# Optimization experiments

Hardware: AMD Instinct MI355X
Metric: run time of the kernel (lower is better)

Reference implementation:

```python
import jax, jax.numpy as jnp
import numpy as np

B = 8192          # batch of scenes
H = 20            # human_num
O = 10            # other_robot_num
IN = 13           # input_dim
SELF = 6          # self_state_dim
AG = IN - SELF    # agent_state_dim = 7
E1, E2 = 256, 128 # wr_dims / wh_dims
HID = 32          # hardcoded hidden_channels in Graphgnn
FIN = 128         # final_state_dim
P1, P2, P3 = 256, 128, 1  # planning_dims
NE = 8            # number of hetero edge types
# edge-type index convention:
# 0 robot->human, 1 human->robot, 2 other->robot, 3 robot->other,
# 4 other->human, 5 human->other, 6 human->human, 7 other->other


def setup_inputs() -> dict:
    key = jax.random.key(0)
    ks = iter(jax.random.split(key, 40))
    def nrm(shape, scale=0.05):
        return jax.random.normal(next(ks), shape, jnp.float32) * scale
    inp = {}
    inp["state"] = jax.random.normal(next(ks), (B, H + O, IN), jnp.float32)
    inp["dropout"] = 0  # unused by forward (kept for signature fidelity)
    # w_r: SELF -> E1 -> E2 (last_relu=True)
    inp["wr_W0"] = nrm((SELF, E1)); inp["wr_b0"] = nrm((E1,))
    inp["wr_W1"] = nrm((E1, E2));   inp["wr_b1"] = nrm((E2,))
    # w_h: AG -> E1 -> E2
    inp["wh_W0"] = nrm((AG, E1));   inp["wh_b0"] = nrm((E1,))
    inp["wh_W1"] = nrm((E1, E2));   inp["wh_b1"] = nrm((E2,))
    # w_o: AG -> E1 -> E2
    inp["wo_W0"] = nrm((AG, E1));   inp["wo_b0"] = nrm((E1,))
    inp["wo_W1"] = nrm((E1, E2));   inp["wo_b1"] = nrm((E2,))
    # per-edge-type GraphConv params (PyG GraphConv: lin_rel has bias, lin_root has none)
    inp["c1_relW"]  = nrm((NE, E2, HID)); inp["c1_relb"]  = nrm((NE, HID))
    inp["c1_rootW"] = nrm((NE, E2, HID))
    inp["c2_relW"]  = nrm((NE, HID, FIN)); inp["c2_relb"]  = nrm((NE, FIN))
    inp["c2_rootW"] = nrm((NE, HID, FIN))
    # value_net: FIN -> P1 -> P2 -> P3 (no final relu)
    inp["v_W0"] = nrm((FIN, P1)); inp["v_b0"] = nrm((P1,))
    inp["v_W1"] = nrm((P1, P2));  inp["v_b1"] = nrm((P2,))
    inp["v_W2"] = nrm((P2, P3));  inp["v_b2"] = nrm((P3,))
    return inp


def _mlp2(x, W0, b0, W1, b1, last_relu):
    h = jax.nn.relu(x @ W0 + b0)
    h = h @ W1 + b1
    return jax.nn.relu(h) if last_relu else h


def _hetero_conv(xr, xh, xo, relW, relb, rootW):
    # xr: [B,1,D], xh: [B,H,D], xo: [B,O,D]
    # GraphConv per edge type: out_dst = lin_root(x_dst) + lin_rel(sum of src messages)
    # graph is complete bipartite (sence) / complete-minus-self (affect),
    # so aggregations are closed-form sums.
    lin  = lambda x, i: jnp.einsum('bnd,do->bno', x, relW[i]) + relb[i]
    root = lambda x, i: jnp.einsum('bnd,do->bno', x, rootW[i])
    sh = xh.sum(axis=1, keepdims=True)  # [B,1,D] sum over humans
    so = xo.sum(axis=1, keepdims=True)  # [B,1,D] sum over other robots
    # robot receives: human->robot (1), other->robot (2)
    out_r = lin(sh, 1) + root(xr, 1) + lin(so, 2) + root(xr, 2)
    # human receives: robot->human (0), other->human (4), human->human (6)
    out_h = (lin(xr, 0) + root(xh, 0)
             + lin(so, 4) + root(xh, 4)
             + lin(sh - xh, 6) + root(xh, 6))
    # other receives: robot->other (3), human->other (5), other->other (7)
    out_o = (lin(xr, 3) + root(xo, 3)
             + lin(sh, 5) + root(xo, 5)
             + lin(so - xo, 7) + root(xo, 7))
    return out_r, out_h, out_o


def reference(state, dropout,
              wr_W0, wr_b0, wr_W1, wr_b1,
              wh_W0, wh_b0, wh_W1, wh_b1,
              wo_W0, wo_b0, wo_W1, wo_b1,
              c1_relW, c1_relb, c1_rootW,
              c2_relW, c2_relb, c2_rootW,
              v_W0, v_b0, v_W1, v_b1, v_W2, v_b2):
    self_state = state[:, 0, :SELF]          # [B, SELF]
    human_states = state[:, :H, SELF:]       # [B, H, AG]
    other_states = state[:, H:, SELF:]       # [B, O, AG]
    er = _mlp2(self_state, wr_W0, wr_b0, wr_W1, wr_b1, True)[:, None, :]  # [B,1,E2]
    eh = _mlp2(human_states, wh_W0, wh_b0, wh_W1, wh_b1, True)            # [B,H,E2]
    eo = _mlp2(other_states, wo_W0, wo_b0, wo_W1, wo_b1, True)            # [B,O,E2]
    r, h, o = _hetero_conv(er, eh, eo, c1_relW, c1_relb, c1_rootW)
    r, h, o = jax.nn.relu(r), jax.nn.relu(h), jax.nn.relu(o)
    r, h, o = _hetero_conv(r, h, o, c2_relW, c2_relb, c2_rootW)
    r = jax.nn.relu(r)
    hr = r[:, 0, :]                           # robot node per scene, [B, FIN]
    v = jax.nn.relu(hr @ v_W0 + v_b0)
    v = jax.nn.relu(v @ v_W1 + v_b1)
    v = v @ v_W2 + v_b2                       # [B, 1]
    return v
```

## Files before the change

kernel.cpp:

```cpp
#include <hip/hip_runtime.h>
#include <hip/hip_bf16.h>
#include <stdint.h>

#define BATCH 8192
#define NSTATE 30
#define DIN 13
#define E1 256
#define E2 128

typedef short bf16x8 __attribute__((ext_vector_type(8)));
typedef float f32x4 __attribute__((ext_vector_type(4)));

__device__ __forceinline__ unsigned short f2b(float f) {
    unsigned u = __float_as_uint(f);
    u += 0x7FFFu + ((u >> 16) & 1u);
    return (unsigned short)(u >> 16);
}
__device__ __forceinline__ float b2f(unsigned short b) {
    return __uint_as_float((unsigned)b << 16);
}
__device__ __forceinline__ unsigned pack2(float a, float b) {
    return ((unsigned)f2b(fmaxf(b, 0.f)) << 16) | f2b(fmaxf(a, 0.f));
}
__device__ __forceinline__ unsigned pack2n(float a, float b) {
    return ((unsigned)f2b(b) << 16) | f2b(a);
}

__device__ __forceinline__ float wcat_val(int k, int m, const float* relW, const float* rootW) {
    int part = k >> 7, c = k & 127, grp = m >> 5, mm = m & 31;
    int off = c * 32 + mm;
    if (part == 0) return (grp == 0) ? rootW[4096 + off] + rootW[8192 + off]
                        : (grp == 1) ? relW[off] : relW[3*4096 + off];
    if (part == 1) return (grp == 0) ? relW[1*4096 + off]
                        : (grp == 1) ? relW[6*4096 + off] : relW[5*4096 + off];
    return (grp == 0) ? relW[2*4096 + off]
         : (grp == 1) ? relW[4*4096 + off] : relW[7*4096 + off];
}
__device__ __forceinline__ float wc2_val(int k, int n, const float* relW, const float* rootW) {
    int grp = k >> 5, kk = k & 31;
    int off = kk * 128 + n;
    if (grp == 0) return rootW[4096 + off] + rootW[8192 + off];
    if (grp == 1) return relW[4096 + off];
    return relW[8192 + off];
}

__global__ void k_prep(const float* __restrict__ c1_relW, const float* __restrict__ c1_relb,
                       const float* __restrict__ c1_rootW,
                       const float* __restrict__ c2_relW, const float* __restrict__ c2_relb,
                       const float* __restrict__ c2_rootW,
                       const float* __restrict__ wh_W0, const float* __restrict__ wh_W1,
                       const float* __restrict__ wo_W0, const float* __restrict__ wo_W1,
                       const float* __restrict__ wr_W0, const float* __restrict__ wr_W1,
                       const float* __restrict__ v_W0, const float* __restrict__ v_W1,
                       float* __restrict__ bcat, float* __restrict__ bc2,
                       unsigned short* __restrict__ W0b_h, unsigned short* __restrict__ W0b_o,
                       unsigned short* __restrict__ W0b_r,
                       unsigned short* __restrict__ W1f_h, unsigned short* __restrict__ W1f_o,
                       unsigned short* __restrict__ W1f_r,
                       unsigned short* __restrict__ Mf_h, unsigned short* __restrict__ Mf_o,
                       unsigned short* __restrict__ Wcatf, unsigned short* __restrict__ Wc2f,
                       unsigned short* __restrict__ vW0f, unsigned short* __restrict__ vW1f)
{
    int gid = blockIdx.x * blockDim.x + threadIdx.x;
    int gsz = gridDim.x * blockDim.x;

    for (int i = gid; i < 96; i += gsz) {
        int grp = i >> 5, mm = i & 31;
        float v;
        if (grp == 0)      v = c1_relb[32 + mm] + c1_relb[64 + mm];
        else if (grp == 1) v = c1_relb[mm] + c1_relb[128 + mm] + c1_relb[192 + mm];
        else               v = c1_relb[96 + mm] + c1_relb[160 + mm] + c1_relb[224 + mm];
        bcat[i] = v;
    }
    for (int i = gid; i < 128; i += gsz) bc2[i] = c2_relb[128 + i] + c2_relb[256 + i];

    for (int i = gid; i < 2048; i += gsz) {
        int n = i >> 3, j = i & 7;
        W0b_h[i] = (j < 7) ? f2b(wh_W0[j * 256 + n]) : 0;
        W0b_o[i] = (j < 7) ? f2b(wo_W0[j * 256 + n]) : 0;
        W0b_r[i] = (j < 6) ? f2b(wr_W0[j * 256 + n]) : 0;
    }
    for (int i = gid; i < 32768; i += gsz) {
        int j = i & 7, l = (i >> 3) & 63, nt = (i >> 9) & 7, ks = i >> 12;
        int k = ks * 32 + (l >> 4) * 8 + j;
        int n = nt * 16 + (l & 15);
        W1f_h[i] = f2b(wh_W1[k * 128 + n]);
        W1f_o[i] = f2b(wo_W1[k * 128 + n]);
        W1f_r[i] = f2b(wr_W1[k * 128 + n]);
    }
    for (int i = gid; i < 4096; i += gsz) {
        int j = i & 7, l = (i >> 3) & 63, nt = (i >> 9) & 1, ks = i >> 10;
        int k = ks * 32 + (l >> 4) * 8 + j;
        int n = nt * 16 + (l & 15);
        int i0 = k * 32 + n;
        Mf_h[i] = f2b(c1_rootW[i0] + c1_rootW[4*4096 + i0] + c1_rootW[6*4096 + i0] - c1_relW[6*4096 + i0]);
        Mf_o[i] = f2b(c1_rootW[3*4096 + i0] + c1_rootW[5*4096 + i0] + c1_rootW[7*4096 + i0] - c1_relW[7*4096 + i0]);
    }
    for (int i = gid; i < 36864; i += gsz) {
        int j = i & 7, l = (i >> 3) & 63, rem = i >> 9;
        int nt = rem % 6, ks = rem / 6;
        int k = ks * 32 + (l >> 4) * 8 + j;
        int n = nt * 16 + (l & 15);
        Wcatf[i] = f2b(wcat_val(k, n, c1_relW, c1_rootW));
    }
    for (int i = gid; i < 12288; i += gsz) {
        int j = i & 7, l = (i >> 3) & 63, rem = i >> 9;
        int nt = rem & 7, ks = rem >> 3;
        int k = ks * 32 + (l >> 4) * 8 + j;
        int n = nt * 16 + (l & 15);
        Wc2f[i] = f2b(wc2_val(k, n, c2_relW, c2_rootW));
    }
    for (int i = gid; i < 32768; i += gsz) {
        int j = i & 7, l = (i >> 3) & 63, rem = i >> 9;
        int nt = rem & 15, ks = rem >> 4;
        int k = ks * 32 + (l >> 4) * 8 + j;
        int n = nt * 16 + (l & 15);
        vW0f[i] = f2b(v_W0[k * 256 + n]);
    }
    for (int i = gid; i < 32768; i += gsz) {
        int j = i & 7, l = (i >> 3) & 63, rem = i >> 9;
        int nt = rem & 7, ks = rem >> 3;
        int k = ks * 32 + (l >> 4) * 8 + j;
        int n = nt * 16 + (l & 15);
        vW1f[i] = f2b(v_W1[k * 128 + n]);
    }
}

#define SM_W0   0
#define SM_MF   4096
#define SM_W1   12288
#define SM_B0   77824
#define SM_B1   78848
#define SM_HS   79360
#define SM_SZ   (79360 + 8 * 16 * 264 * 2)

template<int NPB, int NODE0, int INOFF, int INDIM, bool TAIL>
__device__ __forceinline__ void mlp_blockG(
    int blkrow0, const float* __restrict__ state,
    const unsigned short* __restrict__ W0b_g, const float* __restrict__ b0,
    const unsigned short* __restrict__ W1f_g, const float* __restrict__ b1,
    const unsigned short* __restrict__ Mf_g,
    unsigned short* __restrict__ tR,
    float* __restrict__ sum0, float* __restrict__ sum1,
    unsigned short* __restrict__ eR, char* smem)
{
    unsigned short* W0s = (unsigned short*)(smem + SM_W0);
    unsigned short* Mfs = (unsigned short*)(smem + SM_MF);
    unsigned short* W1s = (unsigned short*)(smem + SM_W1);
    float* b0s          = (float*)(smem + SM_B0);
    float* b1s          = (float*)(smem + SM_B1);

    const int t = threadIdx.x;
    const int lane = t & 63;
    const int w = t >> 6;
    const int l15 = lane & 15;
    const int quad = lane >> 4;
    const int R0 = blkrow0 + w * 128;
    unsigned short* hw = (unsigned short*)(smem + SM_HS) + w * (16 * 264);
    unsigned short* ew = hw;

    if (t < 256) { ((uint4*)W0s)[t] = ((const uint4*)W0b_g)[t]; b0s[t] = b0[t]; }
    if (t >= 256 && t < 384) b1s[t - 256] = b1[t - 256];
    #pragma unroll
    for (int i = 0; i < 8; ++i)
        ((uint4*)W1s)[t + 512 * i] = ((const uint4*)W1f_g)[t + 512 * i];
    if constexpr (TAIL)
        ((uint4*)Mfs)[t] = ((const uint4*)Mf_g)[t];
    __syncthreads();

    float s0 = 0.f, s1 = 0.f;
    int bcur = R0 / NPB;

    for (int sub = 0; sub < 8; ++sub) {
        const int wrow0 = R0 + sub * 16;

        bf16x8 bx = {};
        if (quad == 0) {
            int grow = wrow0 + l15;
            int b = grow / NPB;
            int n = grow - b * NPB + NODE0;
            const float* xp = state + ((size_t)b * NSTATE + n) * DIN + INOFF;
            #pragma unroll
            for (int j = 0; j < INDIM; ++j)
                bx[j] = (short)f2b(xp[j]);
        }

        #pragma unroll
        for (int nt = 0; nt < 16; ++nt) {
            bf16x8 aw = {};
            if (quad == 0)
                aw = *(const bf16x8*)(W0s + (nt * 16 + l15) * 8);
            float4 bb = *(const float4*)(b0s + nt * 16 + quad * 4);
            f32x4 c = {bb.x, bb.y, bb.z, bb.w};
            c = __builtin_amdgcn_mfma_f32_16x16x32_bf16(aw, bx, c, 0, 0, 0);
            uint2 pv = {pack2(c[0], c[1]), pack2(c[2], c[3])};
            *(uint2*)(hw + l15 * 264 + nt * 16 + quad * 4) = pv;
        }

        f32x4 acc[8];
        #pragma unroll
        for (int nt = 0; nt < 8; ++nt) {
            float4 bb = *(const float4*)(b1s + nt * 16 + quad * 4);
            acc[nt] = (f32x4){bb.x, bb.y, bb.z, bb.w};
        }
        #pragma unroll
        for (int ks = 0; ks < 8; ++ks) {
            bf16x8 bh = *(const bf16x8*)(hw + l15 * 264 + ks * 32 + quad * 8);
            #pragma unroll
            for (int nt = 0; nt < 8; ++nt) {
                bf16x8 aw = *(const bf16x8*)(W1s + ((ks * 8 + nt) * 64 + lane) * 8);
                acc[nt] = __builtin_amdgcn_mfma_f32_16x16x32_bf16(aw, bh, acc[nt], 0, 0, 0);
            }
        }

        if constexpr (TAIL) {
            __asm__ __volatile__("s_waitcnt lgkmcnt(0)" ::: "memory");
            #pragma unroll
            for (int nt = 0; nt < 8; ++nt) {
                uint2 pv = {pack2(acc[nt][0], acc[nt][1]), pack2(acc[nt][2], acc[nt][3])};
                *(uint2*)(ew + l15 * 136 + nt * 16 + quad * 4) = pv;
            }

            f32x4 tacc[2] = {{0.f,0.f,0.f,0.f},{0.f,0.f,0.f,0.f}};
            #pragma unroll
            for (int ks = 0; ks < 4; ++ks) {
                bf16x8 ae = *(const bf16x8*)(ew + l15 * 136 + ks * 32 + quad * 8);
                #pragma unroll
                for (int nt = 0; nt < 2; ++nt) {
                    bf16x8 bm = *(const bf16x8*)(Mfs + ((ks * 2 + nt) * 64 + lane) * 8);
                    tacc[nt] = __builtin_amdgcn_mfma_f32_16x16x32_bf16(bm, ae, tacc[nt], 0, 0, 0);
                }
            }
            #pragma unroll
            for (int nt = 0; nt < 2; ++nt) {
                uint2 pv = {pack2n(tacc[nt][0], tacc[nt][1]), pack2n(tacc[nt][2], tacc[nt][3])};
                *(uint2*)(tR + (size_t)(wrow0 + l15) * 32 + nt * 16 + quad * 4) = pv;
            }

            #pragma unroll
            for (int r = 0; r < 16; ++r) {
                int b = (wrow0 + r) / NPB;
                if (b != bcur) {
                    bool head = (bcur * NPB >= R0);
                    float* dst = (head ? sum0 : sum1) + (size_t)bcur * 128 + 2 * lane;
                    dst[0] = s0; dst[1] = s1;
                    s0 = 0.f; s1 = 0.f; bcur = b;
                }
                unsigned v = *(const unsigned*)(ew + r * 136 + lane * 2);
                s0 += b2f((unsigned short)v);
                s1 += b2f((unsigned short)(v >> 16));
            }
            if (sub == 7) {
                bool head = (bcur * NPB >= R0);
                float* dst = (head ? sum0 : sum1) + (size_t)bcur * 128 + 2 * lane;
                dst[0] = s0; dst[1] = s1;
            }
        } else {
            #pragma unroll
            for (int nt = 0; nt < 8; ++nt) {
                uint2 pv = {pack2(acc[nt][0], acc[nt][1]), pack2(acc[nt][2], acc[nt][3])};
                *(uint2*)(eR + (size_t)(wrow0 + l15) * 128 + nt * 16 + quad * 4) = pv;
            }
        }
        __asm__ __volatile__("" ::: "memory");
    }
}

__global__ __launch_bounds__(512, 2) void k_mlpG(
    const float* __restrict__ state,
    const unsigned short* __restrict__ W0b_h, const float* __restrict__ b0_h,
    const unsigned short* __restrict__ W1f_h, const float* __restrict__ b1_h,
    const unsigned short* __restrict__ Mf_h, unsigned short* __restrict__ tR_h,
    float* __restrict__ shB0, float* __restrict__ shB1,
    const unsigned short* __restrict__ W0b_o, const float* __restrict__ b0_o,
    const unsigned short* __restrict__ W1f_o, const float* __restrict__ b1_o,
    const unsigned short* __restrict__ Mf_o, unsigned short* __restrict__ tR_o,
    float* __restrict__ soB0, float* __restrict__ soB1,
    const unsigned short* __restrict__ W0b_r, const float* __restrict__ b0_r,
    const unsigned short* __restrict__ W1f_r, const float* __restrict__ b1_r,
    unsigned short* __restrict__ eR)
{
    __shared__ __align__(16) char smem[SM_SZ];
    int bid = blockIdx.x;
    if (bid < 160)
        mlp_blockG<20, 0, 6, 7, true>(bid * 1024, state, W0b_h, b0_h, W1f_h, b1_h,
                                      Mf_h, tR_h, shB0, shB1, nullptr, smem);
    else if (bid < 240)
        mlp_blockG<10, 20, 6, 7, true>((bid - 160) * 1024, state, W0b_o, b0_o, W1f_o, b1_o,
                                       Mf_o, tR_o, soB0, soB1, nullptr, smem);
    else
        mlp_blockG<1, 0, 0, 6, false>((bid - 240) * 1024, state, W0b_r, b0_r, W1f_r, b1_r,
                                      nullptr, nullptr, nullptr, nullptr, eR, smem);
}

__global__ __launch_bounds__(256, 4) void k_tail(
    const unsigned short* __restrict__ eR,
    const float* __restrict__ shB0, const float* __restrict__ shB1,
    const float* __restrict__ soB0, const float* __restrict__ soB1,
    const unsigned short* __restrict__ tR_h, const unsigned short* __restrict__ tR_o,
    const unsigned short* __restrict__ Wcatf, const float* __restrict__ bcat,
    const unsigned short* __restrict__ Wc2f, const float* __restrict__ bc2,
    const unsigned short* __restrict__ vW0f, const float* __restrict__ vb0,
    const unsigned short* __restrict__ vW1f, const float* __restrict__ vb1,
    const float* __restrict__ vW2, const float* __restrict__ vb2,
    float* __restrict__ out)
{
    __shared__ __align__(16) char sm[33024];
    unsigned short* Ub  = (unsigned short*)(sm);
    unsigned short* V1b = (unsigned short*)(sm);
    unsigned short* Vb  = (unsigned short*)(sm + 12800);
    float* chL          = (float*)(sm + 16128);
    float* coL          = (float*)(sm + 18176);
    unsigned short* Hb  = (unsigned short*)(sm + 20224);
    float* V2b          = (float*)(sm + 24576);

    const int t = threadIdx.x, lane = t & 63, w = t >> 6;
    const int l15 = lane & 15, quad = lane >> 4;
    const int b0 = blockIdx.x * 16;
    const int rowb = quad * 4;

    {
        int b = t >> 4, q = t & 15;
        ((uint4*)(Ub + b * 400))[q] = ((const uint4*)(eR + (size_t)(b0 + b) * 128))[q];
    }
    for (int idx = t; idx < 4096; idx += 256) {
        int b = idx >> 8, kk = idx & 255;
        int bb = b0 + b;
        float v;
        if (kk < 128) {
            v = shB0[(size_t)bb * 128 + kk];
            if (((bb * 20) >> 7) != ((bb * 20 + 19) >> 7))
                v += shB1[(size_t)bb * 128 + kk];
        } else {
            int k2 = kk - 128;
            v = soB0[(size_t)bb * 128 + k2];
            if (((bb * 10) >> 7) != ((bb * 10 + 9) >> 7))
                v += soB1[(size_t)bb * 128 + k2];
        }
        Ub[b * 400 + 128 + kk] = f2b(v);
    }
    __syncthreads();

    for (int nt = w; nt < 6; nt += 4) {
        float bias = bcat[nt * 16 + l15];
        f32x4 acc = {bias, bias, bias, bias};
        #pragma unroll
        for (int ks = 0; ks < 12; ++ks) {
            bf16x8 a = *(const bf16x8*)(Ub + l15 * 400 + ks * 32 + quad * 8);
            bf16x8 bw = *(const bf16x8*)(Wcatf + ((ks * 6 + nt) * 64 + lane) * 8);
            acc = __builtin_amdgcn_mfma_f32_16x16x32_bf16(a, bw, acc, 0, 0, 0);
        }
        int n = nt * 16 + l15;
        #pragma unroll
        for (int reg = 0; reg < 4; ++reg) {
            float v = acc[reg];
            int b = rowb + reg;
            if (n < 32)      Vb[b * 104 + n] = f2b(fmaxf(v, 0.f));
            else if (n < 64) chL[b * 32 + (n - 32)] = v;
            else             coL[b * 32 + (n - 64)] = v;
        }
    }
    __syncthreads();

    for (int idx = t; idx < 512; idx += 256) {
        int b = idx >> 5, m = idx & 31;
        float ch = chL[b * 32 + m];
        const unsigned short* p = tR_h + (size_t)(b0 + b) * 20 * 32 + m;
        float s = 0.f;
        #pragma unroll
        for (int n = 0; n < 20; ++n) s += fmaxf(ch + b2f(p[n * 32]), 0.f);
        Vb[b * 104 + 32 + m] = f2b(s);
        float co = coL[b * 32 + m];
        const unsigned short* p2 = tR_o + (size_t)(b0 + b) * 10 * 32 + m;
        float s2 = 0.f;
        #pragma unroll
        for (int n = 0; n < 10; ++n) s2 += fmaxf(co + b2f(p2[n * 32]), 0.f);
        Vb[b * 104 + 64 + m] = f2b(s2);
    }
    __syncthreads();

    {
        f32x4 acc[2];
        #pragma unroll
        for (int q = 0; q < 2; ++q) {
            int nt = w + q * 4;
            float bias = bc2[nt * 16 + l15];
            acc[q] = (f32x4){bias, bias, bias, bias};
        }
        #pragma unroll
        for (int ks = 0; ks < 3; ++ks) {
            bf16x8 a = *(const bf16x8*)(Vb + l15 * 104 + ks * 32 + quad * 8);
            #pragma unroll
            for (int q = 0; q < 2; ++q) {
                int nt = w + q * 4;
                bf16x8 bw = *(const bf16x8*)(Wc2f + ((ks * 8 + nt) * 64 + lane) * 8);
                acc[q] = __builtin_amdgcn_mfma_f32_16x16x32_bf16(a, bw, acc[q], 0, 0, 0);
            }
        }
        #pragma unroll
        for (int q = 0; q < 2; ++q) {
            int nt = w + q * 4;
            #pragma unroll
            for (int reg = 0; reg < 4; ++reg)
                Hb[(rowb + reg) * 136 + nt * 16 + l15] = f2b(fmaxf(acc[q][reg], 0.f));
        }
    }
    __syncthreads();

    {
        f32x4 acc[4];
        #pragma unroll
        for (int q = 0; q < 4; ++q) {
            int nt = w + q * 4;
            float bias = vb0[nt * 16 + l15];
            acc[q] = (f32x4){bias, bias, bias, bias};
        }
        #pragma unroll
        for (int ks = 0; ks < 4; ++ks) {
            bf16x8 a = *(const bf16x8*)(Hb + l15 * 136 + ks * 32 + quad * 8);
            #pragma unroll
            for (int q = 0; q < 4; ++q) {
                int nt = w + q * 4;
                bf16x8 bw = *(const bf16x8*)(vW0f + ((ks * 16 + nt) * 64 + lane) * 8);
                acc[q] = __builtin_amdgcn_mfma_f32_16x16x32_bf16(a, bw, acc[q], 0, 0, 0);
            }
        }
        __syncthreads();
        #pragma unroll
        for (int q = 0; q < 4; ++q) {
            int nt = w + q * 4;
            #pragma unroll
            for (int reg = 0; reg < 4; ++reg)
                V1b[(rowb + reg) * 264 + nt * 16 + l15] = f2b(fmaxf(acc[q][reg], 0.f));
        }
    }
    __syncthreads();

    {
        f32x4 acc[2];
        #pragma unroll
        for (int q = 0; q < 2; ++q) {
            int nt = w + q * 4;
            float bias = vb1[nt * 16 + l15];
            acc[q] = (f32x4){bias, bias, bias, bias};
        }
        #pragma unroll
        for (int ks = 0; ks < 8; ++ks) {
            bf16x8 a = *(const bf16x8*)(V1b + l15 * 264 + ks * 32 + quad * 8);
            #pragma unroll
            for (int q = 0; q < 2; ++q) {
                int nt = w + q * 4;
                bf16x8 bw = *(const bf16x8*)(vW1f + ((ks * 8 + nt) * 64 + lane) * 8);
                acc[q] = __builtin_amdgcn_mfma_f32_16x16x32_bf16(a, bw, acc[q], 0, 0, 0);
            }
        }
        #pragma unroll
        for (int q = 0; q < 2; ++q) {
            int nt = w + q * 4;
            #pragma unroll
            for (int reg = 0; reg < 4; ++reg)
                V2b[(rowb + reg) * 132 + nt * 16 + l15] = fmaxf(acc[q][reg], 0.f);
        }
    }
    __syncthreads();

    if (t < 128) {
        int b = t >> 3, j = t & 7;
        float v = 0.f;
        #pragma unroll
        for (int k = 0; k < 16; ++k)
            v = fmaf(V2b[b * 132 + j * 16 + k], vW2[j * 16 + k], v);
        v += __shfl_down(v, 4, 8);
        v += __shfl_down(v, 2, 8);
        v += __shfl_down(v, 1, 8);
        if (j == 0) out[b0 + b] = v + vb2[0];
    }
}

extern "C" void kernel_launch(void* const* d_in, const int* in_sizes, int n_in,
                              void* d_out, int out_size, void* d_ws, size_t ws_size,
                              hipStream_t stream)
{
    const float* state   = (const float*)d_in[0];
    const float* wr_W0   = (const float*)d_in[2];
    const float* wr_b0   = (const float*)d_in[3];
    const float* wr_W1   = (const float*)d_in[4];
    const float* wr_b1   = (const float*)d_in[5];
    const float* wh_W0   = (const float*)d_in[6];
    const float* wh_b0   = (const float*)d_in[7];
    const float* wh_W1   = (const float*)d_in[8];
    const float* wh_b1   = (const float*)d_in[9];
    const float* wo_W0   = (const float*)d_in[10];
    const float* wo_b0   = (const float*)d_in[11];
    const float* wo_W1   = (const float*)d_in[12];
    const float* wo_b1   = (const float*)d_in[13];
    const float* c1_relW = (const float*)d_in[14];
    const float* c1_relb = (const float*)d_in[15];
    const float* c1_rootW= (const float*)d_in[16];
    const float* c2_relW = (const float*)d_in[17];
    const float* c2_relb = (const float*)d_in[18];
    const float* c2_rootW= (const float*)d_in[19];
    const float* v_W0    = (const float*)d_in[20];
    const float* v_b0    = (const float*)d_in[21];
    const float* v_W1    = (const float*)d_in[22];
    const float* v_b1    = (const float*)d_in[23];
    const float* v_W2    = (const float*)d_in[24];
    const float* v_b2    = (const float*)d_in[25];

    char* ws = (char*)d_ws;
    size_t off = 0;
    auto alloc = [&](size_t bytes) -> char* {
        char* p = ws + off;
        off = (off + bytes + 255) & ~(size_t)255;
        return p;
    };
    float* shB0 = (float*)alloc((size_t)BATCH * 128 * 4);
    float* shB1 = (float*)alloc((size_t)BATCH * 128 * 4);
    float* soB0 = (float*)alloc((size_t)BATCH * 128 * 4);
    float* soB1 = (float*)alloc((size_t)BATCH * 128 * 4);
    unsigned short* tR_h = (unsigned short*)alloc((size_t)163840 * 32 * 2);
    unsigned short* tR_o = (unsigned short*)alloc((size_t)81920 * 32 * 2);
    unsigned short* eR   = (unsigned short*)alloc((size_t)BATCH * 128 * 2);
    float* bcat = (float*)alloc(96 * 4);
    float* bc2  = (float*)alloc(128 * 4);
    unsigned short* W0b_h = (unsigned short*)alloc(2048 * 2);
    unsigned short* W0b_o = (unsigned short*)alloc(2048 * 2);
    unsigned short* W0b_r = (unsigned short*)alloc(2048 * 2);
    unsigned short* W1f_h = (unsigned short*)alloc(32768 * 2);
    unsigned short* W1f_o = (unsigned short*)alloc(32768 * 2);
    unsigned short* W1f_r = (unsigned short*)alloc(32768 * 2);
    unsigned short* Mf_h  = (unsigned short*)alloc(4096 * 2);
    unsigned short* Mf_o  = (unsigned short*)alloc(4096 * 2);
    unsigned short* Wcatf = (unsigned short*)alloc(36864 * 2);
    unsigned short* Wc2f  = (unsigned short*)alloc(12288 * 2);
    unsigned short* vW0f  = (unsigned short*)alloc(32768 * 2);
    unsigned short* vW1f  = (unsigned short*)alloc(32768 * 2);
    (void)ws_size; (void)in_sizes; (void)n_in; (void)out_size;

    k_prep<<<256, 256, 0, stream>>>(c1_relW, c1_relb, c1_rootW, c2_relW, c2_relb, c2_rootW,
                                    wh_W0, wh_W1, wo_W0, wo_W1, wr_W0, wr_W1, v_W0, v_W1,
                                    bcat, bc2, W0b_h, W0b_o, W0b_r, W1f_h, W1f_o, W1f_r,
                                    Mf_h, Mf_o, Wcatf, Wc2f, vW0f, vW1f);

    k_mlpG<<<248, 512, 0, stream>>>(state,
                                    W0b_h, wh_b0, W1f_h, wh_b1, Mf_h, tR_h, shB0, shB1,
                                    W0b_o, wo_b0, W1f_o, wo_b1, Mf_o, tR_o, soB0, soB1,
                                    W0b_r, wr_b0, W1f_r, wr_b1, eR);

    k_tail<<<512, 256, 0, stream>>>(eR, shB0, shB1, soB0, soB1, tR_h, tR_o,
                                    Wcatf, bcat, Wc2f, bc2, vW0f, v_b0, vW1f, v_b1,
                                    v_W2, v_b2, (float*)d_out);
}
```

Measured before the change: 176.7 us.

## Fold weight prep kernel into MLP kernel and convert weights in-block

Removes the separate k_prep launch. Each MLP block now converts its own fp32 weights to bf16 fragment layout directly into shared memory, and 8 extra blocks in the same grid build the tail-kernel tables. This removes one launch and the global round-trip for the MLP weight tables. In exchange, every MLP block redundantly does strided fp32 loads and conversion of the 32K-element W1, which adds per-block prologue work. The k_tail launch bounds were also changed from 4 to 2.

```diff
diff --git a/kernel.cpp b/kernel.cpp
--- a/kernel.cpp
+++ b/kernel.cpp
@@ -44,88 +44,6 @@
     return relW[8192 + off];
 }
 
-__global__ void k_prep(const float* __restrict__ c1_relW, const float* __restrict__ c1_relb,
-                       const float* __restrict__ c1_rootW,
-                       const float* __restrict__ c2_relW, const float* __restrict__ c2_relb,
-                       const float* __restrict__ c2_rootW,
-                       const float* __restrict__ wh_W0, const float* __restrict__ wh_W1,
-                       const float* __restrict__ wo_W0, const float* __restrict__ wo_W1,
-                       const float* __restrict__ wr_W0, const float* __restrict__ wr_W1,
-                       const float* __restrict__ v_W0, const float* __restrict__ v_W1,
-                       float* __restrict__ bcat, float* __restrict__ bc2,
-                       unsigned short* __restrict__ W0b_h, unsigned short* __restrict__ W0b_o,
-                       unsigned short* __restrict__ W0b_r,
-                       unsigned short* __restrict__ W1f_h, unsigned short* __restrict__ W1f_o,
-                       unsigned short* __restrict__ W1f_r,
-                       unsigned short* __restrict__ Mf_h, unsigned short* __restrict__ Mf_o,
-                       unsigned short* __restrict__ Wcatf, unsigned short* __restrict__ Wc2f,
-                       unsigned short* __restrict__ vW0f, unsigned short* __restrict__ vW1f)
-{
-    int gid = blockIdx.x * blockDim.x + threadIdx.x;
-    int gsz = gridDim.x * blockDim.x;
-
-    for (int i = gid; i < 96; i += gsz) {
-        int grp = i >> 5, mm = i & 31;
-        float v;
-        if (grp == 0)      v = c1_relb[32 + mm] + c1_relb[64 + mm];
-        else if (grp == 1) v = c1_relb[mm] + c1_relb[128 + mm] + c1_relb[192 + mm];
-        else               v = c1_relb[96 + mm] + c1_relb[160 + mm] + c1_relb[224 + mm];
-        bcat[i] = v;
-    }
-    for (int i = gid; i < 128; i += gsz) bc2[i] = c2_relb[128 + i] + c2_relb[256 + i];
-
-    for (int i = gid; i < 2048; i += gsz) {
-        int n = i >> 3, j = i & 7;
-        W0b_h[i] = (j < 7) ? f2b(wh_W0[j * 256 + n]) : 0;
-        W0b_o[i] = (j < 7) ? f2b(wo_W0[j * 256 + n]) : 0;
-        W0b_r[i] = (j < 6) ? f2b(wr_W0[j * 256 + n]) : 0;
-    }
-    for (int i = gid; i < 32768; i += gsz) {
-        int j = i & 7, l = (i >> 3) & 63, nt = (i >> 9) & 7, ks = i >> 12;
-        int k = ks * 32 + (l >> 4) * 8 + j;
-        int n = nt * 16 + (l & 15);
-        W1f_h[i] = f2b(wh_W1[k * 128 + n]);
-        W1f_o[i] = f2b(wo_W1[k * 128 + n]);
-        W1f_r[i] = f2b(wr_W1[k * 128 + n]);
-    }
-    for (int i = gid; i < 4096; i += gsz) {
-        int j = i & 7, l = (i >> 3) & 63, nt = (i >> 9) & 1, ks = i >> 10;
-        int k = ks * 32 + (l >> 4) * 8 + j;
-        int n = nt * 16 + (l & 15);
-        int i0 = k * 32 + n;
-        Mf_h[i] = f2b(c1_rootW[i0] + c1_rootW[4*4096 + i0] + c1_rootW[6*4096 + i0] - c1_relW[6*4096 + i0]);
-        Mf_o[i] = f2b(c1_rootW[3*4096 + i0] + c1_rootW[5*4096 + i0] + c1_rootW[7*4096 + i0] - c1_relW[7*4096 + i0]);
-    }
-    for (int i = gid; i < 36864; i += gsz) {
-        int j = i & 7, l = (i >> 3) & 63, rem = i >> 9;
-        int nt = rem % 6, ks = rem / 6;
-        int k = ks * 32 + (l >> 4) * 8 + j;
-        int n = nt * 16 + (l & 15);
-        Wcatf[i] = f2b(wcat_val(k, n, c1_relW, c1_rootW));
-    }
-    for (int i = gid; i < 12288; i += gsz) {
-        int j = i & 7, l = (i >> 3) & 63, rem = i >> 9;
-        int nt = rem & 7, ks = rem >> 3;
-        int k = ks * 32 + (l >> 4) * 8 + j;
-        int n = nt * 16 + (l & 15);
-        Wc2f[i] = f2b(wc2_val(k, n, c2_relW, c2_rootW));
-    }
-    for (int i = gid; i < 32768; i += gsz) {
-        int j = i & 7, l = (i >> 3) & 63, rem = i >> 9;
-        int nt = rem & 15, ks = rem >> 4;
-        int k = ks * 32 + (l >> 4) * 8 + j;
-        int n = nt * 16 + (l & 15);
-        vW0f[i] = f2b(v_W0[k * 256 + n]);
-    }
-    for (int i = gid; i < 32768; i += gsz) {
-        int j = i & 7, l = (i >> 3) & 63, rem = i >> 9;
-        int nt = rem & 7, ks = rem >> 3;
-        int k = ks * 32 + (l >> 4) * 8 + j;
-        int n = nt * 16 + (l & 15);
-        vW1f[i] = f2b(v_W1[k * 128 + n]);
-    }
-}
-
 #define SM_W0   0
 #define SM_MF   4096
 #define SM_W1   12288
@@ -135,11 +53,12 @@
 #define SM_SZ   (79360 + 8 * 16 * 264 * 2)
 
 template<int NPB, int NODE0, int INOFF, int INDIM, bool TAIL>
-__device__ __forceinline__ void mlp_blockG(
+__device__ __forceinline__ void mlp_blockH(
     int blkrow0, const float* __restrict__ state,
-    const unsigned short* __restrict__ W0b_g, const float* __restrict__ b0,
-    const unsigned short* __restrict__ W1f_g, const float* __restrict__ b1,
-    const unsigned short* __restrict__ Mf_g,
+    const float* __restrict__ W0_raw, const float* __restrict__ b0,
+    const float* __restrict__ W1_raw, const float* __restrict__ b1,
+    const float* __restrict__ c1_relW, const float* __restrict__ c1_rootW,
+    int mo0, int mo1, int mo2, int mrl,
     unsigned short* __restrict__ tR,
     float* __restrict__ sum0, float* __restrict__ sum1,
     unsigned short* __restrict__ eR, char* smem)
@@ -159,13 +78,28 @@
     unsigned short* hw = (unsigned short*)(smem + SM_HS) + w * (16 * 264);
     unsigned short* ew = hw;
 
-    if (t < 256) { ((uint4*)W0s)[t] = ((const uint4*)W0b_g)[t]; b0s[t] = b0[t]; }
-    if (t >= 256 && t < 384) b1s[t - 256] = b1[t - 256];
-    #pragma unroll
-    for (int i = 0; i < 8; ++i)
-        ((uint4*)W1s)[t + 512 * i] = ((const uint4*)W1f_g)[t + 512 * i];
-    if constexpr (TAIL)
-        ((uint4*)Mfs)[t] = ((const uint4*)Mf_g)[t];
+    for (int e = t; e < 2048; e += 512) {
+        int n = e >> 3, j = e & 7;
+        W0s[e] = (j < INDIM) ? f2b(W0_raw[j * 256 + n]) : (unsigned short)0;
+    }
+    if (t < 256) b0s[t] = b0[t];
+    else if (t < 384) b1s[t - 256] = b1[t - 256];
+    for (int e = t; e < 32768; e += 512) {
+        int j = e & 7, l = (e >> 3) & 63, nt = (e >> 9) & 7, ks = e >> 12;
+        int k = ks * 32 + (l >> 4) * 8 + j;
+        int n = nt * 16 + (l & 15);
+        W1s[e] = f2b(W1_raw[k * 128 + n]);
+    }
+    if constexpr (TAIL) {
+        for (int e = t; e < 4096; e += 512) {
+            int j = e & 7, l = (e >> 3) & 63, nt = (e >> 9) & 1, ks = e >> 10;
+            int k = ks * 32 + (l >> 4) * 8 + j;
+            int n = nt * 16 + (l & 15);
+            int i0 = k * 32 + n;
+            Mfs[e] = f2b(c1_rootW[mo0 + i0] + c1_rootW[mo1 + i0] + c1_rootW[mo2 + i0]
+                         - c1_relW[mrl + i0]);
+        }
+    }
     __syncthreads();
 
     float s0 = 0.f, s1 = 0.f;
@@ -266,34 +200,99 @@
     }
 }
 
-__global__ __launch_bounds__(512, 2) void k_mlpG(
+__device__ void prep_tail_tables(
+    int gid, int gsz,
+    const float* __restrict__ c1_relW, const float* __restrict__ c1_relb,
+    const float* __restrict__ c1_rootW,
+    const float* __restrict__ c2_relW, const float* __restrict__ c2_relb,
+    const float* __restrict__ c2_rootW,
+    const float* __restrict__ v_W0, const float* __restrict__ v_W1,
+    float* __restrict__ bcat, float* __restrict__ bc2,
+    unsigned short* __restrict__ Wcatf, unsigned short* __restrict__ Wc2f,
+    unsigned short* __restrict__ vW0f, unsigned short* __restrict__ vW1f)
+{
+    for (int i = gid; i < 96; i += gsz) {
+        int grp = i >> 5, mm = i & 31;
+        float v;
+        if (grp == 0)      v = c1_relb[32 + mm] + c1_relb[64 + mm];
+        else if (grp == 1) v = c1_relb[mm] + c1_relb[128 + mm] + c1_relb[192 + mm];
+        else               v = c1_relb[96 + mm] + c1_relb[160 + mm] + c1_relb[224 + mm];
+        bcat[i] = v;
+    }
+    for (int i = gid; i < 128; i += gsz) bc2[i] = c2_relb[128 + i] + c2_relb[256 + i];
+    for (int i = gid; i < 36864; i += gsz) {
+        int j = i & 7, l = (i >> 3) & 63, rem = i >> 9;
+        int nt = rem % 6, ks = rem / 6;
+        int k = ks * 32 + (l >> 4) * 8 + j;
+        int n = nt * 16 + (l & 15);
+        Wcatf[i] = f2b(wcat_val(k, n, c1_relW, c1_rootW));
+    }
+    for (int i = gid; i < 12288; i += gsz) {
+        int j = i & 7, l = (i >> 3) & 63, rem = i >> 9;
+        int nt = rem & 7, ks = rem >> 3;
+        int k = ks * 32 + (l >> 4) * 8 + j;
+        int n = nt * 16 + (l & 15);
+        Wc2f[i] = f2b(wc2_val(k, n, c2_relW, c2_rootW));
+    }
+    for (int i = gid; i < 32768; i += gsz) {
+        int j = i & 7, l = (i >> 3) & 63, rem = i >> 9;
+        int nt = rem & 15, ks = rem >> 4;
+        int k = ks * 32 + (l >> 4) * 8 + j;
+        int n = nt * 16 + (l & 15);
+        vW0f[i] = f2b(v_W0[k * 256 + n]);
+    }
+    for (int i = gid; i < 32768; i += gsz) {
+        int j = i & 7, l = (i >> 3) & 63, rem = i >> 9;
+        int nt = rem & 7, ks = rem >> 3;
+        int k = ks * 32 + (l >> 4) * 8 + j;
+        int n = nt * 16 + (l & 15);
+        vW1f[i] = f2b(v_W1[k * 128 + n]);
+    }
+}
+
+__global__ __launch_bounds__(512, 2) void k_mlpH(
     const float* __restrict__ state,
-    const unsigned short* __restrict__ W0b_h, const float* __restrict__ b0_h,
-    const unsigned short* __restrict__ W1f_h, const float* __restrict__ b1_h,
-    const unsigned short* __restrict__ Mf_h, unsigned short* __restrict__ tR_h,
+    const float* __restrict__ wh_W0, const float* __restrict__ b0_h,
+    const float* __restrict__ wh_W1, const float* __restrict__ b1_h,
+    unsigned short* __restrict__ tR_h,
     float* __restrict__ shB0, float* __restrict__ shB1,
-    const unsigned short* __restrict__ W0b_o, const float* __restrict__ b0_o,
-    const unsigned short* __restrict__ W1f_o, const float* __restrict__ b1_o,
-    const unsigned short* __restrict__ Mf_o, unsigned short* __restrict__ tR_o,
+    const float* __restrict__ wo_W0, const float* __restrict__ b0_o,
+    const float* __restrict__ wo_W1, const float* __restrict__ b1_o,
+    unsigned short* __restrict__ tR_o,
     float* __restrict__ soB0, float* __restrict__ soB1,
-    const unsigned short* __restrict__ W0b_r, const float* __restrict__ b0_r,
-    const unsigned short* __restrict__ W1f_r, const float* __restrict__ b1_r,
-    unsigned short* __restrict__ eR)
+    const float* __restrict__ wr_W0, const float* __restrict__ b0_r,
+    const float* __restrict__ wr_W1, const float* __restrict__ b1_r,
+    unsigned short* __restrict__ eR,
+    const float* __restrict__ c1_relW, const float* __restrict__ c1_relb,
+    const float* __restrict__ c1_rootW,
+    const float* __restrict__ c2_relW, const float* __restrict__ c2_relb,
+    const float* __restrict__ c2_rootW,
+    const float* __restrict__ v_W0, const float* __restrict__ v_W1,
+    float* __restrict__ bcat, float* __restrict__ bc2,
+    unsigned short* __restrict__ Wcatf, unsigned short* __restrict__ Wc2f,
+    unsigned short* __restrict__ vW0f, unsigned short* __restrict__ vW1f)
 {
     __shared__ __align__(16) char smem[SM_SZ];
     int bid = blockIdx.x;
     if (bid < 160)
-        mlp_blockG<20, 0, 6, 7, true>(bid * 1024, state, W0b_h, b0_h, W1f_h, b1_h,
-                                      Mf_h, tR_h, shB0, shB1, nullptr, smem);
+        mlp_blockH<20, 0, 6, 7, true>(bid * 1024, state, wh_W0, b0_h, wh_W1, b1_h,
+                                      c1_relW, c1_rootW, 0, 4*4096, 6*4096, 6*4096,
+                                      tR_h, shB0, shB1, nullptr, smem);
     else if (bid < 240)
-        mlp_blockG<10, 20, 6, 7, true>((bid - 160) * 1024, state, W0b_o, b0_o, W1f_o, b1_o,
-                                       Mf_o, tR_o, soB0, soB1, nullptr, smem);
+        mlp_blockH<10, 20, 6, 7, true>((bid - 160) * 1024, state, wo_W0, b0_o, wo_W1, b1_o,
+                                       c1_relW, c1_rootW, 3*4096, 5*4096, 7*4096, 7*4096,
+                                       tR_o, soB0, soB1, nullptr, smem);
+    else if (bid < 248)
+        mlp_blockH<1, 0, 0, 6, false>((bid - 240) * 1024, state, wr_W0, b0_r, wr_W1, b1_r,
+                                      c1_relW, c1_rootW, 0, 0, 0, 0,
+                                      nullptr, nullptr, nullptr, eR, smem);
     else
-        mlp_blockG<1, 0, 0, 6, false>((bid - 240) * 1024, state, W0b_r, b0_r, W1f_r, b1_r,
-                                      nullptr, nullptr, nullptr, nullptr, eR, smem);
-}
-
-__global__ __launch_bounds__(256, 4) void k_tail(
+        prep_tail_tables((bid - 248) * 512 + threadIdx.x, 8 * 512,
+                         c1_relW, c1_relb, c1_rootW, c2_relW, c2_relb, c2_rootW,
+                         v_W0, v_W1, bcat, bc2, Wcatf, Wc2f, vW0f, vW1f);
+}
+
+__global__ __launch_bounds__(256, 2) void k_tail(
     const unsigned short* __restrict__ eR,
     const float* __restrict__ shB0, const float* __restrict__ shB1,
     const float* __restrict__ soB0, const float* __restrict__ soB1,
@@ -523,29 +522,19 @@
     unsigned short* eR   = (unsigned short*)alloc((size_t)BATCH * 128 * 2);
     float* bcat = (float*)alloc(96 * 4);
     float* bc2  = (float*)alloc(128 * 4);
-    unsigned short* W0b_h = (unsigned short*)alloc(2048 * 2);
-    unsigned short* W0b_o = (unsigned short*)alloc(2048 * 2);
-    unsigned short* W0b_r = (unsigned short*)alloc(2048 * 2);
-    unsigned short* W1f_h = (unsigned short*)alloc(32768 * 2);
-    unsigned short* W1f_o = (unsigned short*)alloc(32768 * 2);
-    unsigned short* W1f_r = (unsigned short*)alloc(32768 * 2);
-    unsigned short* Mf_h  = (unsigned short*)alloc(4096 * 2);
-    unsigned short* Mf_o  = (unsigned short*)alloc(4096 * 2);
     unsigned short* Wcatf = (unsigned short*)alloc(36864 * 2);
     unsigned short* Wc2f  = (unsigned short*)alloc(12288 * 2);
     unsigned short* vW0f  = (unsigned short*)alloc(32768 * 2);
     unsigned short* vW1f  = (unsigned short*)alloc(32768 * 2);
     (void)ws_size; (void)in_sizes; (void)n_in; (void)out_size;
 
-    k_prep<<<256, 256, 0, stream>>>(c1_relW, c1_relb, c1_rootW, c2_relW, c2_relb, c2_rootW,
-                                    wh_W0, wh_W1, wo_W0, wo_W1, wr_W0, wr_W1, v_W0, v_W1,
-                                    bcat, bc2, W0b_h, W0b_o, W0b_r, W1f_h, W1f_o, W1f_r,
-                                    Mf_h, Mf_o, Wcatf, Wc2f, vW0f, vW1f);
-
-    k_mlpG<<<248, 512, 0, stream>>>(state,
-                                    W0b_h, wh_b0, W1f_h, wh_b1, Mf_h, tR_h, shB0, shB1,
-                                    W0b_o, wo_b0, W1f_o, wo_b1, Mf_o, tR_o, soB0, soB1,
-                                    W0b_r, wr_b0, W1f_r, wr_b1, eR);
+    k_mlpH<<<256, 512, 0, stream>>>(state,
+                                    wh_W0, wh_b0, wh_W1, wh_b1, tR_h, shB0, shB1,
+                                    wo_W0, wo_b0, wo_W1, wo_b1, tR_o, soB0, soB1,
+                                    wr_W0, wr_b0, wr_W1, wr_b1, eR,
+                                    c1_relW, c1_relb, c1_rootW,
+                                    c2_relW, c2_relb, c2_rootW,
+                                    v_W0, v_W1, bcat, bc2, Wcatf, Wc2f, vW0f, vW1f);
 
     k_tail<<<512, 256, 0, stream>>>(eR, shB0, shB1, soB0, soB1, tR_h, tR_o,
                                     Wcatf, bcat, Wc2f, bc2, vW0f, v_b0, vW1f, v_b1,
```

Measured after the change: 179.9 us. About the same (+1.8%).
